# Kernel optimization log

Measured on AMD Instinct MI355X. Metric: run time of the kernel, lower is better.

Reference implementation:

```python
import jax, jax.numpy as jnp
import numpy as np


def setup_inputs() -> dict:
    key = jax.random.key(0)
    ks = jax.random.split(key, 5)
    B, C, W, H = 8, 256, 64, 64
    d = C // 8  # query/key channels per SAGAN k=8
    s = 1.0 / np.sqrt(C)
    return {
        "x": jax.random.normal(ks[0], (B, C, W, H), dtype=jnp.float32),
        "wq": jax.random.normal(ks[1], (d, C), dtype=jnp.float32) * s,
        "bq": jnp.zeros((d,), dtype=jnp.float32),
        "wk": jax.random.normal(ks[2], (d, C), dtype=jnp.float32) * s,
        "bk": jnp.zeros((d,), dtype=jnp.float32),
        "wv": jax.random.normal(ks[3], (C, C), dtype=jnp.float32) * s,
        "bv": jnp.zeros((C,), dtype=jnp.float32),
        # gamma is init to 0 in torch; set to 1 so the attention branch is active
        "gamma": jnp.ones((1,), dtype=jnp.float32),
    }


def reference(x, wq, bq, wk, bk, wv, bv, gamma):
    B, C, W, H = x.shape
    N = W * H
    xf = x.reshape(B, C, N)  # spatial tokens flattened
    # 1x1 convs == per-token channel matmuls
    q = jnp.einsum('dc,bcn->bdn', wq, xf) + bq[None, :, None]  # [B, d, N]
    k = jnp.einsum('dc,bcn->bdn', wk, xf) + bk[None, :, None]  # [B, d, N]
    v = jnp.einsum('ec,bcn->ben', wv, xf) + bv[None, :, None]  # [B, C, N]
    # attention_map[b,i,j] = softmax_j( sum_d k[b,d,i] * q[b,d,j] )
    scores = jnp.einsum('bdi,bdj->bij', k, q)  # [B, N, N]
    attention_map = jax.nn.softmax(scores, axis=-1)
    # attention_out[b,c,n] = sum_m v[b,c,m] * A[b,m,n]
    attention_out = jnp.einsum('bcm,bmn->bcn', v, attention_map).reshape(B, C, W, H)
    out = gamma * attention_out + x
    return out, attention_map
```

## Files before the change

kernel.cpp:

```cpp
#include <hip/hip_runtime.h>

#define B 8
#define C 256
#define NN 4096

typedef float f32x4 __attribute__((ext_vector_type(4)));
typedef short s16x8 __attribute__((ext_vector_type(8)));
typedef unsigned short u16;
typedef unsigned int u32;

__device__ __forceinline__ u16 f2bf(float f) {
    u32 u = __builtin_bit_cast(u32, f);
    u32 r = (u + 0x7fffu + ((u >> 16) & 1u)) >> 16;
    return (u16)r;
}
__device__ __forceinline__ float bf2f(u16 h) {
    u32 u = ((u32)h) << 16;
    return __builtin_bit_cast(float, u);
}

__device__ __forceinline__ void bar_lds() {
    asm volatile("s_waitcnt lgkmcnt(0)\n\ts_barrier" ::: "memory");
}

#define MFMA(a, b, c) __builtin_amdgcn_mfma_f32_16x16x32_bf16((a), (b), (c), 0, 0, 0)

__device__ __forceinline__ f32x4 score_mfma_t(s16x8 aqh, s16x8 aql, s16x8 bkh, s16x8 bkl) {
    f32x4 s = {0.f, 0.f, 0.f, 0.f};
    s = MFMA(aqh, bkl, s);
    s = MFMA(aql, bkh, s);
    s = MFMA(aqh, bkh, s);
    return s;
}

__global__ void k_sentinel(float* __restrict__ out, float v) { out[0] = v; }

__global__ void k_cast(const float* __restrict__ wv, const float* __restrict__ wq,
                       const float* __restrict__ wk, u16* __restrict__ wvb,
                       u16* __restrict__ wqh, u16* __restrict__ wql,
                       u16* __restrict__ wkh, u16* __restrict__ wkl) {
    int i = blockIdx.x * 256 + threadIdx.x;
    if (i < 65536) {
        int e = i & 7, lan = (i >> 3) & 15, g = (i >> 7) & 3, ck = (i >> 9) & 7, es = i >> 12;
        wvb[i] = f2bf(wv[(es * 16 + lan) * 256 + ck * 32 + g * 8 + e]);
    } else if (i < 73728) {
        int j = i - 65536;
        int e = j & 7, lan = (j >> 3) & 15, g = (j >> 7) & 3, ck = (j >> 9) & 7, es = j >> 12;
        float v = wq[(es * 16 + lan) * 256 + ck * 32 + g * 8 + e];
        u16 h = f2bf(v); wqh[j] = h; wql[j] = f2bf(v - bf2f(h));
    } else {
        int j = i - 73728;
        int e = j & 7, lan = (j >> 3) & 15, g = (j >> 7) & 3, ck = (j >> 9) & 7, es = j >> 12;
        float v = wk[(es * 16 + lan) * 256 + ck * 32 + g * 8 + e];
        u16 h = f2bf(v); wkh[j] = h; wkl[j] = f2bf(v - bf2f(h));
    }
}

__global__ __launch_bounds__(256) void k_proj(
    const float* __restrict__ x,
    const u16* __restrict__ wvb, const float* __restrict__ bv,
    const u16* __restrict__ wqh, const u16* __restrict__ wql, const float* __restrict__ bq,
    const u16* __restrict__ wkh, const u16* __restrict__ wkl, const float* __restrict__ bk,
    u16* __restrict__ vbf,
    u16* __restrict__ qh, u16* __restrict__ ql, u16* __restrict__ kh, u16* __restrict__ kl)
{
    __shared__ u16 smh[64 * 264];
    __shared__ u16 sml[64 * 264];
    int t = threadIdx.x;
    int w = t >> 6, l = t & 63;
    int lan = l & 15, g = l >> 4;
    int b = blockIdx.x, nblk = blockIdx.y;
    int n0 = nblk * 64;
#pragma unroll
    for (int p = 0; p < 16; p++) {
        int flat4 = t + p * 256;
        int c = flat4 >> 4, n4 = (flat4 & 15) * 4;
        float4 xv = *(const float4*)&x[((size_t)b * C + c) * NN + n0 + n4];
        float vv[4] = {xv.x, xv.y, xv.z, xv.w};
#pragma unroll
        for (int j = 0; j < 4; j++) {
            u16 h = f2bf(vv[j]);
            smh[(n4 + j) * 264 + c] = h;
            sml[(n4 + j) * 264 + c] = f2bf(vv[j] - bf2f(h));
        }
    }
    __syncthreads();
    f32x4 accv[16];
    f32x4 accq[2], acck[2];
#pragma unroll
    for (int es = 0; es < 16; es++) accv[es] = {0.f, 0.f, 0.f, 0.f};
#pragma unroll
    for (int es = 0; es < 2; es++) { accq[es] = {0.f, 0.f, 0.f, 0.f}; acck[es] = {0.f, 0.f, 0.f, 0.f}; }
    int nrow = w * 16 + lan;
    for (int ck = 0; ck < 8; ck++) {
        int c0 = ck * 32 + g * 8;
        int fb = ((ck * 4 + g) * 16 + lan) * 8;
        s16x8 bh = *(const s16x8*)&smh[nrow * 264 + c0];
        s16x8 bl = *(const s16x8*)&sml[nrow * 264 + c0];
#pragma unroll
        for (int es = 0; es < 16; es++) {
            s16x8 afrag = *(const s16x8*)&wvb[es * 4096 + fb];
            accv[es] = MFMA(afrag, bh, accv[es]);
        }
#pragma unroll
        for (int es = 0; es < 2; es++) {
            s16x8 ah = *(const s16x8*)&wqh[es * 4096 + fb];
            s16x8 al = *(const s16x8*)&wql[es * 4096 + fb];
            accq[es] = MFMA(ah, bl, accq[es]);
            accq[es] = MFMA(al, bh, accq[es]);
            accq[es] = MFMA(ah, bh, accq[es]);
            ah = *(const s16x8*)&wkh[es * 4096 + fb];
            al = *(const s16x8*)&wkl[es * 4096 + fb];
            acck[es] = MFMA(ah, bl, acck[es]);
            acck[es] = MFMA(al, bh, acck[es]);
            acck[es] = MFMA(ah, bh, acck[es]);
        }
    }
    int ncol = n0 + w * 16 + lan;
#pragma unroll
    for (int es = 0; es < 16; es++)
#pragma unroll
        for (int r = 0; r < 4; r++) {
            int e = es * 16 + g * 4 + r;
            vbf[((size_t)b * C + e) * NN + ncol] = f2bf(accv[es][r] + bv[e]);
        }
    bar_lds();
    u16* sqk = sml;
    int nloc = w * 16 + lan;
#pragma unroll
    for (int es = 0; es < 2; es++)
#pragma unroll
        for (int r = 0; r < 4; r++) {
            int d = es * 16 + g * 4 + r;
            float qv = accq[es][r] + bq[d];
            float kv = acck[es][r] + bk[d];
            u16 qhi = f2bf(qv); u16 qlo = f2bf(qv - bf2f(qhi));
            u16 khi = f2bf(kv); u16 klo = f2bf(kv - bf2f(khi));
            sqk[nloc * 136 + 0 * 32 + d] = qhi;
            sqk[nloc * 136 + 1 * 32 + d] = qlo;
            sqk[nloc * 136 + 2 * 32 + d] = khi;
            sqk[nloc * 136 + 3 * 32 + d] = klo;
        }
    bar_lds();
    {
        int n = t >> 2, arr = t & 3;
        const u16* src = &sqk[n * 136 + arr * 32];
        u16* dst = (arr == 0 ? qh : arr == 1 ? ql : arr == 2 ? kh : kl) + ((size_t)b * NN + n0 + n) * 32;
        uint4 v0 = *(const uint4*)&src[0];
        uint4 v1 = *(const uint4*)&src[8];
        uint4 v2 = *(const uint4*)&src[16];
        uint4 v3 = *(const uint4*)&src[24];
        *(uint4*)&dst[0]  = v0;
        *(uint4*)&dst[8]  = v1;
        *(uint4*)&dst[16] = v2;
        *(uint4*)&dst[24] = v3;
    }
}

__global__ __launch_bounds__(256) void k_zsum(
    const u16* __restrict__ qh, const u16* __restrict__ ql,
    const u16* __restrict__ kh, const u16* __restrict__ kl,
    float* __restrict__ zinv)
{
    __shared__ float lZ[4][64];
    int t = threadIdx.x;
    int w = t >> 6, l = t & 63;
    int lan = l & 15, g = l >> 4;
    int b = blockIdx.x, mblk = blockIdx.y;
    int m0 = mblk * 64;

    s16x8 bkh[4], bkl[4];
#pragma unroll
    for (int ms = 0; ms < 4; ms++) {
        size_t ko = ((size_t)b * NN + m0 + ms * 16 + lan) * 32 + g * 8;
        bkh[ms] = *(const s16x8*)&kh[ko];
        bkl[ms] = *(const s16x8*)&kl[ko];
    }
    float zacc[4] = {0.f, 0.f, 0.f, 0.f};
    for (int ci = 0; ci < 64; ci++) {
        int nt = ci * 4 + w;
        size_t qo = ((size_t)b * NN + nt * 16 + lan) * 32 + g * 8;
        s16x8 aqh = *(const s16x8*)&qh[qo];
        s16x8 aql = *(const s16x8*)&ql[qo];
#pragma unroll
        for (int ms = 0; ms < 4; ms++) {
            f32x4 s = score_mfma_t(aqh, aql, bkh[ms], bkl[ms]);
            zacc[ms] += __expf(s[0]) + __expf(s[1]) + __expf(s[2]) + __expf(s[3]);
        }
    }
#pragma unroll
    for (int ms = 0; ms < 4; ms++) {
        float v = zacc[ms];
        v += __shfl_xor(v, 16);
        v += __shfl_xor(v, 32);
        zacc[ms] = v;
    }
    if (g == 0) {
#pragma unroll
        for (int ms = 0; ms < 4; ms++) lZ[w][ms * 16 + lan] = zacc[ms];
    }
    __syncthreads();
    if (t < 64) {
        float Z = lZ[0][t] + lZ[1][t] + lZ[2][t] + lZ[3][t];
        zinv[(size_t)b * NN + m0 + t] = 1.0f / Z;
    }
}

__global__ __launch_bounds__(256) void k_attn2(
    const float* __restrict__ x,
    const u16* __restrict__ qh, const u16* __restrict__ ql,
    const u16* __restrict__ kh, const u16* __restrict__ kl,
    const u16* __restrict__ vbf, const float* __restrict__ zinv,
    const float* __restrict__ gamma,
    float* __restrict__ out, float* __restrict__ amap)
{
    __shared__ u16 smv[16384];
    __shared__ u16 mn[64 * 68];
    __shared__ u16 nm[64 * 80];
    int t = threadIdx.x;
    int w = t >> 6, l = t & 63;
    int lan = l & 15, g = l >> 4;
    int b = blockIdx.x, nblk = blockIdx.y;
    int n0 = nblk * 64;
    int nw = n0 + w * 16;

    size_t qo = ((size_t)b * NN + nw + lan) * 32 + g * 8;
    s16x8 aqh = *(const s16x8*)&qh[qo];
    s16x8 aql = *(const s16x8*)&ql[qo];

    f32x4 acc[4][4];
#pragma unroll
    for (int ct = 0; ct < 4; ct++)
#pragma unroll
        for (int nt = 0; nt < 4; nt++) acc[ct][nt] = {0.f, 0.f, 0.f, 0.f};

    const u16* vb = vbf + (size_t)b * C * NN;
    const float* ziv = zinv + (size_t)b * NN;
    float* amp = amap + (size_t)b * NN * NN;

    s16x8 vreg[8];
#pragma unroll
    for (int p = 0; p < 8; p++) {
        int f8 = t + p * 256; int c = f8 >> 3, j = f8 & 7;
        vreg[p] = *(const s16x8*)&vb[(size_t)c * NN + j * 8];
    }
#pragma unroll
    for (int p = 0; p < 8; p++) {
        int f8 = t + p * 256; int c = f8 >> 3, j = f8 & 7;
        *(s16x8*)&smv[c * 64 + ((j ^ (c & 7)) * 8)] = vreg[p];
    }
    bar_lds();

    for (int mstep = 0; mstep < 64; mstep++) {
        int m0 = mstep * 64;
#pragma unroll
        for (int ms = 0; ms < 4; ms++) {
            size_t ko = ((size_t)b * NN + m0 + ms * 16 + lan) * 32 + g * 8;
            s16x8 fkh = *(const s16x8*)&kh[ko];
            s16x8 fkl = *(const s16x8*)&kl[ko];
            f32x4 s = score_mfma_t(aqh, aql, fkh, fkl);
            float zi = ziv[m0 + ms * 16 + lan];
            u16 b0 = f2bf(__expf(s[0]) * zi);
            u16 b1 = f2bf(__expf(s[1]) * zi);
            u16 b2 = f2bf(__expf(s[2]) * zi);
            u16 b3 = f2bf(__expf(s[3]) * zi);
            uint2 pk;
            pk.x = (u32)b0 | ((u32)b1 << 16);
            pk.y = (u32)b2 | ((u32)b3 << 16);
            *(uint2*)&mn[(ms * 16 + lan) * 68 + w * 16 + g * 4] = pk;
            int nr = w * 16 + g * 4;
            nm[(nr + 0) * 80 + ms * 16 + lan] = b0;
            nm[(nr + 1) * 80 + ms * 16 + lan] = b1;
            nm[(nr + 2) * 80 + ms * 16 + lan] = b2;
            nm[(nr + 3) * 80 + ms * 16 + lan] = b3;
        }
        bar_lds();
        if (mstep < 63) {
#pragma unroll
            for (int p = 0; p < 8; p++) {
                int f8 = t + p * 256; int c = f8 >> 3, j = f8 & 7;
                vreg[p] = *(const s16x8*)&vb[(size_t)c * NN + m0 + 64 + j * 8];
            }
        }
#pragma unroll
        for (int p = 0; p < 4; p++) {
            int mm = p * 16 + (t >> 4);
            int c4 = (t & 15) * 4;
            uint2 pk = *(const uint2*)&mn[mm * 68 + c4];
            f32x4 v;
            v[0] = bf2f((u16)(pk.x & 0xffff)); v[1] = bf2f((u16)(pk.x >> 16));
            v[2] = bf2f((u16)(pk.y & 0xffff)); v[3] = bf2f((u16)(pk.y >> 16));
            __builtin_nontemporal_store(v, (f32x4*)&amp[(size_t)(m0 + mm) * NN + n0 + c4]);
        }
#pragma unroll
        for (int ks = 0; ks < 2; ks++) {
            s16x8 bfr[4];
#pragma unroll
            for (int nt = 0; nt < 4; nt++)
                bfr[nt] = *(const s16x8*)&nm[(nt * 16 + lan) * 80 + ks * 32 + g * 8];
#pragma unroll
            for (int ct = 0; ct < 4; ct++) {
                int row = w * 64 + ct * 16 + lan;
                s16x8 af = *(const s16x8*)&smv[row * 64 + (((ks * 4 + g) ^ (lan & 7)) * 8)];
#pragma unroll
                for (int nt = 0; nt < 4; nt++)
                    acc[ct][nt] = MFMA(af, bfr[nt], acc[ct][nt]);
            }
        }
        bar_lds();
        if (mstep < 63) {
#pragma unroll
            for (int p = 0; p < 8; p++) {
                int f8 = t + p * 256; int c = f8 >> 3, j = f8 & 7;
                *(s16x8*)&smv[c * 64 + ((j ^ (c & 7)) * 8)] = vreg[p];
            }
        }
    }
    float gm = gamma[0];
#pragma unroll
    for (int ct = 0; ct < 4; ct++)
#pragma unroll
        for (int nt = 0; nt < 4; nt++)
#pragma unroll
            for (int r = 0; r < 4; r++) {
                int c = w * 64 + ct * 16 + g * 4 + r;
                size_t oi = ((size_t)b * C + c) * NN + n0 + nt * 16 + lan;
                out[oi] = gm * acc[ct][nt][r] + x[oi];
            }
}

extern "C" void kernel_launch(void* const* d_in, const int* in_sizes, int n_in,
                              void* d_out, int out_size, void* d_ws, size_t ws_size,
                              hipStream_t stream) {
    const float* x     = (const float*)d_in[0];
    const float* wq    = (const float*)d_in[1];
    const float* bq    = (const float*)d_in[2];
    const float* wk    = (const float*)d_in[3];
    const float* bk    = (const float*)d_in[4];
    const float* wv    = (const float*)d_in[5];
    const float* bv    = (const float*)d_in[6];
    const float* gamma = (const float*)d_in[7];
    float* out  = (float*)d_out;
    float* amap = out + (size_t)B * C * NN;

    const size_t WS_NEED = (size_t)26 << 20;
    if (ws_size < WS_NEED) {
        k_sentinel<<<dim3(1), dim3(1), 0, stream>>>(out, 8.0e7f);
        return;
    }
    if (n_in < 8 || in_sizes[0] != B * C * NN || in_sizes[1] != 32 * C ||
        in_sizes[2] != 32 || in_sizes[3] != 32 * C || in_sizes[4] != 32 ||
        in_sizes[5] != C * C || in_sizes[6] != C || in_sizes[7] != 1) {
        k_sentinel<<<dim3(1), dim3(1), 0, stream>>>(out, 9.0e7f);
        return;
    }

    unsigned char* ws = (unsigned char*)d_ws;
    u16* qh   = (u16*)(ws);
    u16* ql   = (u16*)(ws + ((size_t)2 << 20));
    u16* kh   = (u16*)(ws + ((size_t)4 << 20));
    u16* kl   = (u16*)(ws + ((size_t)6 << 20));
    u16* vbf  = (u16*)(ws + ((size_t)8 << 20));
    float* zinv = (float*)(ws + ((size_t)24 << 20));
    u16* wvb  = (u16*)(ws + ((size_t)25 << 20));
    u16* wqh  = (u16*)(ws + ((size_t)25 << 20) + (128 << 10));
    u16* wql  = (u16*)(ws + ((size_t)25 << 20) + (144 << 10));
    u16* wkh  = (u16*)(ws + ((size_t)25 << 20) + (160 << 10));
    u16* wkl  = (u16*)(ws + ((size_t)25 << 20) + (176 << 10));

    k_cast<<<dim3(320), dim3(256), 0, stream>>>(wv, wq, wk, wvb, wqh, wql, wkh, wkl);
    k_proj<<<dim3(8, 64), dim3(256), 0, stream>>>(x, wvb, bv, wqh, wql, bq, wkh, wkl, bk,
                                                  vbf, qh, ql, kh, kl);
    k_zsum<<<dim3(8, 64), dim3(256), 0, stream>>>(qh, ql, kh, kl, zinv);
    k_attn2<<<dim3(8, 64), dim3(256), 0, stream>>>(x, qh, ql, kh, kl, vbf, zinv, gamma, out, amap);
}
```

Baseline: 290.2 us.

## Double-buffer attention tiles and make V staging wave-private to drop a barrier

Each wave now loads and swizzles only the 64 V channel rows it consumes, so V staging in shared memory no longer needs a block-wide barrier. The probability tiles (mn/nm) are double-buffered by iteration parity, which removes the second per-step barrier. The nm row pitch changes from 80 to 72, and wave priority is raised around the MFMA block to favour matrix issue. This costs extra LDS for the second buffer, and bank-conflict behaviour may change with the new padding.

```diff
diff --git a/kernel.cpp b/kernel.cpp
--- a/kernel.cpp
+++ b/kernel.cpp
@@ -215,8 +215,8 @@
     float* __restrict__ out, float* __restrict__ amap)
 {
     __shared__ u16 smv[16384];
-    __shared__ u16 mn[64 * 68];
-    __shared__ u16 nm[64 * 80];
+    __shared__ u16 mn[2][64 * 68];
+    __shared__ u16 nm[2][64 * 72];
     int t = threadIdx.x;
     int w = t >> 6, l = t & 63;
     int lan = l & 15, g = l >> 4;
@@ -241,18 +241,19 @@
     s16x8 vreg[8];
 #pragma unroll
     for (int p = 0; p < 8; p++) {
-        int f8 = t + p * 256; int c = f8 >> 3, j = f8 & 7;
-        vreg[p] = *(const s16x8*)&vb[(size_t)c * NN + j * 8];
+        int u = l + p * 64; int cl = u >> 3, j = u & 7;
+        vreg[p] = *(const s16x8*)&vb[(size_t)(w * 64 + cl) * NN + j * 8];
     }
 #pragma unroll
     for (int p = 0; p < 8; p++) {
-        int f8 = t + p * 256; int c = f8 >> 3, j = f8 & 7;
-        *(s16x8*)&smv[c * 64 + ((j ^ (c & 7)) * 8)] = vreg[p];
-    }
-    bar_lds();
+        int u = l + p * 64; int cl = u >> 3, j = u & 7;
+        *(s16x8*)&smv[(w * 64 + cl) * 64 + ((j ^ (cl & 7)) * 8)] = vreg[p];
+    }
 
     for (int mstep = 0; mstep < 64; mstep++) {
         int m0 = mstep * 64;
+        u16* mnc = mn[mstep & 1];
+        u16* nmc = nm[mstep & 1];
 #pragma unroll
         for (int ms = 0; ms < 4; ms++) {
             size_t ko = ((size_t)b * NN + m0 + ms * 16 + lan) * 32 + g * 8;
@@ -267,37 +268,38 @@
             uint2 pk;
             pk.x = (u32)b0 | ((u32)b1 << 16);
             pk.y = (u32)b2 | ((u32)b3 << 16);
-            *(uint2*)&mn[(ms * 16 + lan) * 68 + w * 16 + g * 4] = pk;
+            *(uint2*)&mnc[(ms * 16 + lan) * 68 + w * 16 + g * 4] = pk;
             int nr = w * 16 + g * 4;
-            nm[(nr + 0) * 80 + ms * 16 + lan] = b0;
-            nm[(nr + 1) * 80 + ms * 16 + lan] = b1;
-            nm[(nr + 2) * 80 + ms * 16 + lan] = b2;
-            nm[(nr + 3) * 80 + ms * 16 + lan] = b3;
+            nmc[(nr + 0) * 72 + ms * 16 + lan] = b0;
+            nmc[(nr + 1) * 72 + ms * 16 + lan] = b1;
+            nmc[(nr + 2) * 72 + ms * 16 + lan] = b2;
+            nmc[(nr + 3) * 72 + ms * 16 + lan] = b3;
         }
         bar_lds();
         if (mstep < 63) {
 #pragma unroll
             for (int p = 0; p < 8; p++) {
-                int f8 = t + p * 256; int c = f8 >> 3, j = f8 & 7;
-                vreg[p] = *(const s16x8*)&vb[(size_t)c * NN + m0 + 64 + j * 8];
+                int u = l + p * 64; int cl = u >> 3, j = u & 7;
+                vreg[p] = *(const s16x8*)&vb[(size_t)(w * 64 + cl) * NN + m0 + 64 + j * 8];
             }
         }
 #pragma unroll
         for (int p = 0; p < 4; p++) {
             int mm = p * 16 + (t >> 4);
             int c4 = (t & 15) * 4;
-            uint2 pk = *(const uint2*)&mn[mm * 68 + c4];
+            uint2 pk = *(const uint2*)&mnc[mm * 68 + c4];
             f32x4 v;
             v[0] = bf2f((u16)(pk.x & 0xffff)); v[1] = bf2f((u16)(pk.x >> 16));
             v[2] = bf2f((u16)(pk.y & 0xffff)); v[3] = bf2f((u16)(pk.y >> 16));
             __builtin_nontemporal_store(v, (f32x4*)&amp[(size_t)(m0 + mm) * NN + n0 + c4]);
         }
+        __builtin_amdgcn_s_setprio(1);
 #pragma unroll
         for (int ks = 0; ks < 2; ks++) {
             s16x8 bfr[4];
 #pragma unroll
             for (int nt = 0; nt < 4; nt++)
-                bfr[nt] = *(const s16x8*)&nm[(nt * 16 + lan) * 80 + ks * 32 + g * 8];
+                bfr[nt] = *(const s16x8*)&nmc[(nt * 16 + lan) * 72 + ks * 32 + g * 8];
 #pragma unroll
             for (int ct = 0; ct < 4; ct++) {
                 int row = w * 64 + ct * 16 + lan;
@@ -307,12 +309,12 @@
                     acc[ct][nt] = MFMA(af, bfr[nt], acc[ct][nt]);
             }
         }
-        bar_lds();
+        __builtin_amdgcn_s_setprio(0);
         if (mstep < 63) {
 #pragma unroll
             for (int p = 0; p < 8; p++) {
-                int f8 = t + p * 256; int c = f8 >> 3, j = f8 & 7;
-                *(s16x8*)&smv[c * 64 + ((j ^ (c & 7)) * 8)] = vreg[p];
+                int u = l + p * 64; int cl = u >> 3, j = u & 7;
+                *(s16x8*)&smv[(w * 64 + cl) * 64 + ((j ^ (cl & 7)) * 8)] = vreg[p];
             }
         }
     }
```

Result: faster. 272.2 us (-6.2%).
